# Optimization experiments

Measured on AMD Instinct MI355X. Metric: run time of the kernel, lower is better.

## Reference

```python
import jax, jax.numpy as jnp
import numpy as np

NUM_EXPERTS = 8
TOP_K = 2
DIM = 1024
HIDDEN = 4096
BATCH, SEQ = 16, 32


def setup_inputs() -> dict:
    key = jax.random.key(0)
    k1, k2, k3, k4, k5 = jax.random.split(key, 5)
    scale = 1.0 / np.sqrt(DIM)
    return {
        "hidden_states": jax.random.normal(k1, (BATCH, SEQ, DIM), dtype=jnp.float32),
        "gate_w": jax.random.normal(k2, (NUM_EXPERTS, DIM), dtype=jnp.float32) * scale,
        "w1": jax.random.normal(k3, (NUM_EXPERTS, HIDDEN, DIM), dtype=jnp.float32) * scale,
        "w3": jax.random.normal(k4, (NUM_EXPERTS, HIDDEN, DIM), dtype=jnp.float32) * scale,
        "w2": jax.random.normal(k5, (NUM_EXPERTS, DIM, HIDDEN), dtype=jnp.float32) * (1.0 / np.sqrt(HIDDEN)),
    }


def reference(hidden_states, gate_w, w1, w3, w2):
    B, S, D = hidden_states.shape
    x = hidden_states.reshape(-1, D)  # [T, D]

    # Router: softmax in fp32, top-k, renormalize (Mixtral style)
    router_logits = x @ gate_w.T  # [T, E]
    probs = jax.nn.softmax(router_logits.astype(jnp.float32), axis=-1)
    routing_weights, selected_experts = jax.lax.top_k(probs, TOP_K)  # [T, K]
    routing_weights = routing_weights / routing_weights.sum(axis=-1, keepdims=True)
    routing_weights = routing_weights.astype(x.dtype)

    # Per-token per-expert combine coefficient: coef[t, e] = sum_k w[t,k] * 1[sel[t,k]==e]
    coef = (jax.nn.one_hot(selected_experts, NUM_EXPERTS, dtype=x.dtype)
            * routing_weights[..., None]).sum(axis=1)  # [T, E]

    # SwiGLU FFN for all experts (grouped GEMM form), combined by coef.
    h1 = jnp.einsum('td,ehd->teh', x, w1)           # [T, E, H]
    h3 = jnp.einsum('td,ehd->teh', x, w3)           # [T, E, H]
    act = jax.nn.silu(h1) * h3                      # [T, E, H]
    expert_out = jnp.einsum('teh,edh->ted', act, w2)  # [T, E, D]
    out = jnp.einsum('ted,te->td', expert_out, coef)  # [T, D]
    return out.reshape(B, S, D)
```

## Files before the change

kernel.cpp:

```cpp
#include <hip/hip_runtime.h>
#include <hip/hip_bf16.h>

#define E_ 8
#define D_ 1024
#define H_ 4096
#define T_ 512
#define A_ 1024
#define BM_ 192

typedef __attribute__((ext_vector_type(8))) short bf16x8;
typedef __attribute__((ext_vector_type(4))) float f32x4;

__device__ __forceinline__ unsigned short f2bf(float f) {
  __hip_bfloat16 h = __float2bfloat16(f);
  return *reinterpret_cast<unsigned short*>(&h);
}

__device__ __forceinline__ bf16x8 pk8(float4 a, float4 b) {
  bf16x8 r;
  r[0] = (short)f2bf(a.x); r[1] = (short)f2bf(a.y);
  r[2] = (short)f2bf(a.z); r[3] = (short)f2bf(a.w);
  r[4] = (short)f2bf(b.x); r[5] = (short)f2bf(b.y);
  r[6] = (short)f2bf(b.z); r[7] = (short)f2bf(b.w);
  return r;
}

__device__ __forceinline__ void gl16(const void* g, void* l) {
  __builtin_amdgcn_global_load_lds(
      (const __attribute__((address_space(1))) unsigned int*)g,
      (__attribute__((address_space(3))) unsigned int*)l, 16, 0, 0);
}

__global__ void moe_router(const float* __restrict__ x,
                           const float* __restrict__ gw,
                           unsigned short* __restrict__ xb,
                           int* __restrict__ sel,
                           float* __restrict__ wtop) {
  const int t = blockIdx.x;
  const int lane = threadIdx.x;
  const float* xr = x + (size_t)t * D_;

  float4 xv[4];
#pragma unroll
  for (int i = 0; i < 4; ++i) xv[i] = *reinterpret_cast<const float4*>(xr + (i * 64 + lane) * 4);
#pragma unroll
  for (int i = 0; i < 4; ++i) {
    ushort4 u;
    u.x = f2bf(xv[i].x); u.y = f2bf(xv[i].y); u.z = f2bf(xv[i].z); u.w = f2bf(xv[i].w);
    *reinterpret_cast<ushort4*>(xb + (size_t)t * D_ + (i * 64 + lane) * 4) = u;
  }

  float lg[E_];
  for (int e = 0; e < E_; ++e) {
    const float* g = gw + (size_t)e * D_;
    float p = 0.f;
#pragma unroll
    for (int i = 0; i < 4; ++i) {
      float4 gv = *reinterpret_cast<const float4*>(g + (i * 64 + lane) * 4);
      p += xv[i].x * gv.x + xv[i].y * gv.y + xv[i].z * gv.z + xv[i].w * gv.w;
    }
#pragma unroll
    for (int off = 32; off; off >>= 1) p += __shfl_xor(p, off);
    lg[e] = p;
  }
  if (lane == 0) {
    float m = lg[0];
    for (int e = 1; e < E_; ++e) m = fmaxf(m, lg[e]);
    float pr[E_];
    float s = 0.f;
    for (int e = 0; e < E_; ++e) { pr[e] = __expf(lg[e] - m); s += pr[e]; }
    const float inv = 1.f / s;
    for (int e = 0; e < E_; ++e) pr[e] *= inv;
    float v0 = -1.f, v1 = -1.f; int i0 = 0, i1 = 0;
    for (int e = 0; e < E_; ++e) {
      float p = pr[e];
      if (p > v0)      { v1 = v0; i1 = i0; v0 = p; i0 = e; }
      else if (p > v1) { v1 = p; i1 = e; }
    }
    const float s2 = 1.f / (v0 + v1);
    sel[2 * t] = i0; sel[2 * t + 1] = i1;
    wtop[2 * t] = v0 * s2; wtop[2 * t + 1] = v1 * s2;
  }
}

__global__ void moe_compact(const int* __restrict__ sel,
                            const float* __restrict__ wtop,
                            int* __restrict__ counts,
                            int* __restrict__ offsets,
                            int* __restrict__ tok,
                            int* __restrict__ slotof,
                            float* __restrict__ coef) {
  const int tid = threadIdx.x;
  const int e = tid >> 6;
  const int lane = tid & 63;
  __shared__ int cnt[E_], offs[E_];

  int base = 0;
  for (int c = 0; c < T_ / 64; ++c) {
    const int t = c * 64 + lane;
    const bool f = (sel[2 * t] == e) || (sel[2 * t + 1] == e);
    base += __popcll(__ballot(f));
  }
  if (lane == 0) cnt[e] = base;
  __syncthreads();
  if (tid == 0) {
    int o = 0;
    for (int i = 0; i < E_; ++i) { offs[i] = o; o += cnt[i]; }
  }
  __syncthreads();
  if (lane == 0) { counts[e] = cnt[e]; offsets[e] = offs[e]; }

  int pos = offs[e];
  for (int c = 0; c < T_ / 64; ++c) {
    const int t = c * 64 + lane;
    const int s0 = sel[2 * t], s1 = sel[2 * t + 1];
    const bool f = (s0 == e) || (s1 == e);
    unsigned long long b = __ballot(f);
    const int myp = pos + __popcll(b & ((1ull << lane) - 1ull));
    if (f) {
      const int k = (s0 == e) ? 0 : 1;
      tok[myp] = t;
      slotof[2 * t + k] = myp;
      coef[myp] = wtop[2 * t + k];
    }
    pos += __popcll(b);
  }
}


#define STAGE1(buf, kt) do {                                                  \
    _Pragma("unroll")                                                         \
    for (int j = 0; j < 3; ++j)                                               \
      gl16(asrc[j] + (kt), &As[buf][(j * 4 + wid) * 512]);                    \
    _Pragma("unroll")                                                         \
    for (int j = 0; j < 2; ++j) {                                             \
      gl16(b1src[j] + (kt), &B1s[buf][(j * 4 + wid) * 256]);                  \
      gl16(b3src[j] + (kt), &B3s[buf][(j * 4 + wid) * 256]);                  \
    }                                                                         \
  } while (0)

__launch_bounds__(256, 2)
__global__ void moe_ffn1(const unsigned short* __restrict__ xb,
                         const float* __restrict__ w1,
                         const float* __restrict__ w3,
                         const int* __restrict__ counts,
                         const int* __restrict__ offsets,
                         const int* __restrict__ tok,
                         unsigned short* __restrict__ act) {
  const int bid = blockIdx.x;
  const int hg = bid & 63;
  const int e = bid >> 6;
  const int count = counts[e];
  const int off = offsets[e];
  const int hbase = hg * 64;

  __shared__ unsigned short As[2][BM_ * 32];
  __shared__ float B1s[2][64 * 32];
  __shared__ float B3s[2][64 * 32];

  const int tid = threadIdx.x;
  const int lane = tid & 63, wid = tid >> 6;
  const int lr = lane & 15, kg = lane >> 4;
  const int wm = wid * 48;

  const int cA = (((lane & 3) ^ ((lane >> 3) & 3)) << 3);
  const int cB = (((lane & 7) ^ ((lane >> 3) & 7)) << 2);
  const float* b1src[2];
  const float* b3src[2];
#pragma unroll
  for (int j = 0; j < 2; ++j) {
    const int row = (j * 4 + wid) * 8 + (lane >> 3);
    b1src[j] = w1 + ((size_t)e * H_ + hbase + row) * D_ + cB;
    b3src[j] = w3 + ((size_t)e * H_ + hbase + row) * D_ + cB;
  }

  for (int m0 = 0; m0 < count; m0 += BM_) {
    const unsigned short* asrc[3];
#pragma unroll
    for (int j = 0; j < 3; ++j) {
      const int row = (j * 4 + wid) * 16 + (lane >> 2);
      const int cr = (m0 + row < count) ? (m0 + row) : (count - 1);
      asrc[j] = xb + (size_t)tok[off + cr] * D_ + cA;
    }
    const int q = count - m0 - wm;
    const int mfn = (q <= 0) ? 0 : ((q + 15) >> 4 < 3 ? (q + 15) >> 4 : 3);

    f32x4 acc1[3][4] = {};
    f32x4 acc3[3][4] = {};

    STAGE1(0, 0);
    __syncthreads();

    int cur = 0;
    const int pa = ((kg ^ ((lr >> 1) & 3)) << 3);
    const int q0 = (((kg * 2) ^ (lr & 7)) << 2);
    const int q1 = (((kg * 2 + 1) ^ (lr & 7)) << 2);
    for (int it = 0; it < 32; ++it) {
      if (it + 1 < 32) STAGE1(cur ^ 1, (it + 1) * 32);
      bf16x8 af[3];
#pragma unroll
      for (int mf = 0; mf < 3; ++mf)
        af[mf] = *reinterpret_cast<const bf16x8*>(&As[cur][(wm + mf * 16 + lr) * 32 + pa]);
#pragma unroll
      for (int nf = 0; nf < 4; ++nf) {
        const int rb = (nf * 16 + lr) * 32;
        bf16x8 b1f = pk8(*reinterpret_cast<const float4*>(&B1s[cur][rb + q0]),
                         *reinterpret_cast<const float4*>(&B1s[cur][rb + q1]));
        bf16x8 b3f = pk8(*reinterpret_cast<const float4*>(&B3s[cur][rb + q0]),
                         *reinterpret_cast<const float4*>(&B3s[cur][rb + q1]));
#pragma unroll
        for (int mf = 0; mf < 3; ++mf)
          if (mf < mfn) {
            acc1[mf][nf] = __builtin_amdgcn_mfma_f32_16x16x32_bf16(af[mf], b1f, acc1[mf][nf], 0, 0, 0);
            acc3[mf][nf] = __builtin_amdgcn_mfma_f32_16x16x32_bf16(af[mf], b3f, acc3[mf][nf], 0, 0, 0);
          }
      }
      if (it + 1 < 32) { __syncthreads(); cur ^= 1; }
    }

#pragma unroll
    for (int mf = 0; mf < 3; ++mf) {
#pragma unroll
      for (int r = 0; r < 4; ++r) {
        const int mrow = m0 + wm + mf * 16 + kg * 4 + r;
        if (mrow < count) {
          const size_t rb = (size_t)(off + mrow) * H_;
#pragma unroll
          for (int nf = 0; nf < 4; ++nf) {
            const float h1 = acc1[mf][nf][r];
            const float h3 = acc3[mf][nf][r];
            const float a = h1 / (1.f + __expf(-h1)) * h3;
            act[rb + hbase + nf * 16 + lr] = f2bf(a);
          }
        }
      }
    }
    __syncthreads();
  }
}

#define STAGE2(buf, kt) do {                                                  \
    _Pragma("unroll")                                                         \
    for (int j = 0; j < 3; ++j)                                               \
      gl16(asrc[j] + (kt), &As[buf][(j * 4 + wid) * 512]);                    \
    _Pragma("unroll")                                                         \
    for (int j = 0; j < 2; ++j)                                               \
      gl16(bsrc[j] + (kt), &Bs[buf][(j * 4 + wid) * 256]);                    \
  } while (0)

__launch_bounds__(256, 2)
__global__ void moe_ffn2(const unsigned short* __restrict__ act,
                         const float* __restrict__ w2,
                         const int* __restrict__ counts,
                         const int* __restrict__ offsets,
                         const float* __restrict__ coef,
                         float* __restrict__ part,
                         int kschunk) {
  const int bid = blockIdx.x;
  const int ks = bid >> 7;
  const int e = (bid >> 4) & 7;
  const int dg = bid & 15;
  const int count = counts[e];
  const int off = offsets[e];
  const int dbase = dg * 64;
  const int kbase = ks * kschunk;
  const int nit = kschunk >> 5;

  __shared__ unsigned short As[2][BM_ * 32];
  __shared__ float Bs[2][64 * 32];

  const int tid = threadIdx.x;
  const int lane = tid & 63, wid = tid >> 6;
  const int lr = lane & 15, kg = lane >> 4;
  const int wm = wid * 48;

  const int cA = (((lane & 3) ^ ((lane >> 3) & 3)) << 3);
  const int cB = (((lane & 7) ^ ((lane >> 3) & 7)) << 2);
  const float* bsrc[2];
#pragma unroll
  for (int j = 0; j < 2; ++j) {
    const int row = (j * 4 + wid) * 8 + (lane >> 3);
    bsrc[j] = w2 + ((size_t)e * D_ + dbase + row) * H_ + kbase + cB;
  }

  for (int m0 = 0; m0 < count; m0 += BM_) {
    const unsigned short* asrc[3];
#pragma unroll
    for (int j = 0; j < 3; ++j) {
      const int row = (j * 4 + wid) * 16 + (lane >> 2);
      const int cr = (m0 + row < count) ? (m0 + row) : (count - 1);
      asrc[j] = act + (size_t)(off + cr) * H_ + kbase + cA;
    }
    const int q = count - m0 - wm;
    const int mfn = (q <= 0) ? 0 : ((q + 15) >> 4 < 3 ? (q + 15) >> 4 : 3);

    f32x4 acc[3][4] = {};

    STAGE2(0, 0);
    __syncthreads();

    int cur = 0;
    const int pa = ((kg ^ ((lr >> 1) & 3)) << 3);
    const int q0 = (((kg * 2) ^ (lr & 7)) << 2);
    const int q1 = (((kg * 2 + 1) ^ (lr & 7)) << 2);
    for (int it = 0; it < nit; ++it) {
      if (it + 1 < nit) STAGE2(cur ^ 1, (it + 1) * 32);
      bf16x8 af[3];
#pragma unroll
      for (int mf = 0; mf < 3; ++mf)
        af[mf] = *reinterpret_cast<const bf16x8*>(&As[cur][(wm + mf * 16 + lr) * 32 + pa]);
#pragma unroll
      for (int nf = 0; nf < 4; ++nf) {
        const int rb = (nf * 16 + lr) * 32;
        bf16x8 bf = pk8(*reinterpret_cast<const float4*>(&Bs[cur][rb + q0]),
                        *reinterpret_cast<const float4*>(&Bs[cur][rb + q1]));
#pragma unroll
        for (int mf = 0; mf < 3; ++mf)
          if (mf < mfn)
            acc[mf][nf] = __builtin_amdgcn_mfma_f32_16x16x32_bf16(af[mf], bf, acc[mf][nf], 0, 0, 0);
      }
      if (it + 1 < nit) { __syncthreads(); cur ^= 1; }
    }

#pragma unroll
    for (int mf = 0; mf < 3; ++mf) {
#pragma unroll
      for (int r = 0; r < 4; ++r) {
        const int mrow = m0 + wm + mf * 16 + kg * 4 + r;
        if (mrow < count) {
          const float cf = coef[off + mrow];
          float* prow = part + ((size_t)ks * A_ + off + mrow) * D_;
#pragma unroll
          for (int nf = 0; nf < 4; ++nf)
            prow[dbase + nf * 16 + lr] = cf * acc[mf][nf][r];
        }
      }
    }
    __syncthreads();
  }
}

__global__ void moe_combine(const float* __restrict__ part,
                            const int* __restrict__ slotof,
                            float* __restrict__ out,
                            int ksn) {
  const int t = blockIdx.x;
  const int i = threadIdx.x;
  const int g0 = slotof[2 * t], g1 = slotof[2 * t + 1];
  float4 o = make_float4(0.f, 0.f, 0.f, 0.f);
  for (int ks = 0; ks < ksn; ++ks) {
    const float* p = part + (size_t)ks * A_ * D_;
    float4 a = reinterpret_cast<const float4*>(p + (size_t)g0 * D_)[i];
    float4 b = reinterpret_cast<const float4*>(p + (size_t)g1 * D_)[i];
    o.x += a.x + b.x; o.y += a.y + b.y; o.z += a.z + b.z; o.w += a.w + b.w;
  }
  reinterpret_cast<float4*>(out + (size_t)t * D_)[i] = o;
}

extern "C" void kernel_launch(void* const* d_in, const int* in_sizes, int n_in,
                              void* d_out, int out_size, void* d_ws, size_t ws_size,
                              hipStream_t stream) {
  const float* x  = (const float*)d_in[0];
  const float* gw = (const float*)d_in[1];
  const float* w1 = (const float*)d_in[2];
  const float* w3 = (const float*)d_in[3];
  const float* w2 = (const float*)d_in[4];
  float* out = (float*)d_out;

  char* ws = (char*)d_ws;
  const size_t SM   = 32768;
  const size_t ACT  = (size_t)A_ * H_ * 2;
  const size_t XB   = (size_t)T_ * D_ * 2;
  const size_t P1   = (size_t)A_ * D_ * 4;

  char* sm = ws;
  unsigned short* act = (unsigned short*)(ws + SM);
  unsigned short* xb  = (unsigned short*)(ws + SM + ACT);
  float* part         = (float*)(ws + SM + ACT + XB);
  const size_t base = SM + ACT + XB;
  const int ksn = (ws_size >= base + 4 * P1) ? 4 : (ws_size >= base + 2 * P1) ? 2 : 1;

  int*   sel     = (int*)  (sm);
  float* wtop    = (float*)(sm + 4096);
  int*   counts  = (int*)  (sm + 8192);
  int*   offsets = (int*)  (sm + 8192 + 64);
  int*   tokl    = (int*)  (sm + 12288);
  int*   slotof  = (int*)  (sm + 16384);
  float* coef    = (float*)(sm + 20480);

  moe_router <<<T_, 64, 0, stream>>>(x, gw, xb, sel, wtop);
  moe_compact<<<1, 512, 0, stream>>>(sel, wtop, counts, offsets, tokl, slotof, coef);
  moe_ffn1   <<<E_ * 64, 256, 0, stream>>>(xb, w1, w3, counts, offsets, tokl, act);
  moe_ffn2   <<<128 * ksn, 256, 0, stream>>>(act, w2, counts, offsets, coef, part, H_ / ksn);
  moe_combine<<<T_, 256, 0, stream>>>(part, slotof, out, ksn);
}
```

Before: 144.9 us.

## Triple-buffer weight tiles, load activations directly to registers, interleave experts

Both FFN kernels stop staging the activation/token tile in shared memory. Each lane now reads its A fragments straight from global memory into registers. Weight tiles use a 3-stage ring buffer with manual vmcnt waits and a single barrier per iteration, replacing the double buffer with two syncthreads. Block indexing is changed so adjacent blocks belong to different experts, occupancy bounds are raised, and ffn2 may use 8 K-splits when workspace allows. The risks are hand-counted vmcnt values that could race if the compiler reorders loads, uncoalesced direct A reads, and a larger partial buffer for combine to reduce.

```diff
diff --git a/kernel.cpp b/kernel.cpp
--- a/kernel.cpp
+++ b/kernel.cpp
@@ -7,6 +7,7 @@
 #define T_ 512
 #define A_ 1024
 #define BM_ 192
+#define NBUF 3
 
 typedef __attribute__((ext_vector_type(8))) short bf16x8;
 typedef __attribute__((ext_vector_type(4))) float f32x4;
@@ -128,18 +129,21 @@
 }
 
 
-#define STAGE1(buf, kt) do {                                                  \
-    _Pragma("unroll")                                                         \
-    for (int j = 0; j < 3; ++j)                                               \
-      gl16(asrc[j] + (kt), &As[buf][(j * 4 + wid) * 512]);                    \
-    _Pragma("unroll")                                                         \
-    for (int j = 0; j < 2; ++j) {                                             \
-      gl16(b1src[j] + (kt), &B1s[buf][(j * 4 + wid) * 256]);                  \
-      gl16(b3src[j] + (kt), &B3s[buf][(j * 4 + wid) * 256]);                  \
-    }                                                                         \
+#define WAITS(it, nit)                                                        \
+    if ((it) == 0)              asm volatile("s_waitcnt vmcnt(4)" ::: "memory"); \
+    else if ((it) == (nit) - 1) asm volatile("s_waitcnt vmcnt(3)" ::: "memory"); \
+    else                        asm volatile("s_waitcnt vmcnt(7)" ::: "memory"); \
+    __builtin_amdgcn_s_barrier();                                             \
+    __builtin_amdgcn_sched_barrier(0);
+
+#define STAGE1(s, kt) do {                                                    \
+    gl16(b1src[0] + (kt), &B1s[s][wid * 256]);                                \
+    gl16(b1src[1] + (kt), &B1s[s][1024 + wid * 256]);                         \
+    gl16(b3src[0] + (kt), &B3s[s][wid * 256]);                                \
+    gl16(b3src[1] + (kt), &B3s[s][1024 + wid * 256]);                         \
   } while (0)
 
-__launch_bounds__(256, 2)
+__launch_bounds__(256, 3)
 __global__ void moe_ffn1(const unsigned short* __restrict__ xb,
                          const float* __restrict__ w1,
                          const float* __restrict__ w3,
@@ -148,23 +152,21 @@
                          const int* __restrict__ tok,
                          unsigned short* __restrict__ act) {
   const int bid = blockIdx.x;
-  const int hg = bid & 63;
-  const int e = bid >> 6;
+  const int e = bid & 7;
+  const int hg = bid >> 3;
   const int count = counts[e];
   const int off = offsets[e];
   const int hbase = hg * 64;
 
-  __shared__ unsigned short As[2][BM_ * 32];
-  __shared__ float B1s[2][64 * 32];
-  __shared__ float B3s[2][64 * 32];
+  __shared__ float B1s[NBUF][64 * 32];
+  __shared__ float B3s[NBUF][64 * 32];
 
   const int tid = threadIdx.x;
   const int lane = tid & 63, wid = tid >> 6;
   const int lr = lane & 15, kg = lane >> 4;
   const int wm = wid * 48;
 
-  const int cA = (((lane & 3) ^ ((lane >> 3) & 3)) << 3);
-  const int cB = (((lane & 7) ^ ((lane >> 3) & 7)) << 2);
+  const int cB = (((lane & 7) ^ (lane >> 3)) << 2);
   const float* b1src[2];
   const float* b3src[2];
 #pragma unroll
@@ -173,34 +175,40 @@
     b1src[j] = w1 + ((size_t)e * H_ + hbase + row) * D_ + cB;
     b3src[j] = w3 + ((size_t)e * H_ + hbase + row) * D_ + cB;
   }
+  const int q0 = (((2 * kg) ^ (lr & 7)) << 2);
+  const int q1 = (((2 * kg + 1) ^ (lr & 7)) << 2);
 
   for (int m0 = 0; m0 < count; m0 += BM_) {
-    const unsigned short* asrc[3];
-#pragma unroll
-    for (int j = 0; j < 3; ++j) {
-      const int row = (j * 4 + wid) * 16 + (lane >> 2);
-      const int cr = (m0 + row < count) ? (m0 + row) : (count - 1);
-      asrc[j] = xb + (size_t)tok[off + cr] * D_ + cA;
-    }
-    const int q = count - m0 - wm;
-    const int mfn = (q <= 0) ? 0 : ((q + 15) >> 4 < 3 ? (q + 15) >> 4 : 3);
+    const unsigned short* ap[3];
+#pragma unroll
+    for (int mf = 0; mf < 3; ++mf) {
+      const int row = m0 + wm + mf * 16 + lr;
+      const int cr = (row < count) ? row : (count - 1);
+      ap[mf] = xb + (size_t)tok[off + cr] * D_ + kg * 8;
+    }
+    const int qq = count - m0 - wm;
+    const int mfn = (qq <= 0) ? 0 : ((qq + 15) >> 4 < 3 ? (qq + 15) >> 4 : 3);
 
     f32x4 acc1[3][4] = {};
     f32x4 acc3[3][4] = {};
 
     STAGE1(0, 0);
-    __syncthreads();
+    STAGE1(1, 32);
 
     int cur = 0;
-    const int pa = ((kg ^ ((lr >> 1) & 3)) << 3);
-    const int q0 = (((kg * 2) ^ (lr & 7)) << 2);
-    const int q1 = (((kg * 2 + 1) ^ (lr & 7)) << 2);
     for (int it = 0; it < 32; ++it) {
-      if (it + 1 < 32) STAGE1(cur ^ 1, (it + 1) * 32);
+      WAITS(it, 32);
+
       bf16x8 af[3];
 #pragma unroll
       for (int mf = 0; mf < 3; ++mf)
-        af[mf] = *reinterpret_cast<const bf16x8*>(&As[cur][(wm + mf * 16 + lr) * 32 + pa]);
+        af[mf] = *reinterpret_cast<const bf16x8*>(ap[mf] + it * 32);
+
+      if (it + 2 < 32) {
+        int s2 = cur + 2; if (s2 >= NBUF) s2 -= NBUF;
+        STAGE1(s2, (it + 2) * 32);
+      }
+
 #pragma unroll
       for (int nf = 0; nf < 4; ++nf) {
         const int rb = (nf * 16 + lr) * 32;
@@ -215,7 +223,7 @@
             acc3[mf][nf] = __builtin_amdgcn_mfma_f32_16x16x32_bf16(af[mf], b3f, acc3[mf][nf], 0, 0, 0);
           }
       }
-      if (it + 1 < 32) { __syncthreads(); cur ^= 1; }
+      ++cur; if (cur >= NBUF) cur -= NBUF;
     }
 
 #pragma unroll
@@ -239,16 +247,12 @@
   }
 }
 
-#define STAGE2(buf, kt) do {                                                  \
-    _Pragma("unroll")                                                         \
-    for (int j = 0; j < 3; ++j)                                               \
-      gl16(asrc[j] + (kt), &As[buf][(j * 4 + wid) * 512]);                    \
-    _Pragma("unroll")                                                         \
-    for (int j = 0; j < 2; ++j)                                               \
-      gl16(bsrc[j] + (kt), &Bs[buf][(j * 4 + wid) * 256]);                    \
+#define STAGE2(s, kt) do {                                                    \
+    gl16(bsrc[0] + (kt), &Bs[s][wid * 256]);                                  \
+    gl16(bsrc[1] + (kt), &Bs[s][1024 + wid * 256]);                           \
   } while (0)
 
-__launch_bounds__(256, 2)
+__launch_bounds__(256, 4)
 __global__ void moe_ffn2(const unsigned short* __restrict__ act,
                          const float* __restrict__ w2,
                          const int* __restrict__ counts,
@@ -257,58 +261,63 @@
                          float* __restrict__ part,
                          int kschunk) {
   const int bid = blockIdx.x;
-  const int ks = bid >> 7;
-  const int e = (bid >> 4) & 7;
-  const int dg = bid & 15;
+  const int e = bid & 7;
+  const int r2 = bid >> 3;
+  const int dg = r2 & 15;
+  const int ks = r2 >> 4;
   const int count = counts[e];
   const int off = offsets[e];
   const int dbase = dg * 64;
   const int kbase = ks * kschunk;
   const int nit = kschunk >> 5;
 
-  __shared__ unsigned short As[2][BM_ * 32];
-  __shared__ float Bs[2][64 * 32];
+  __shared__ float Bs[NBUF][64 * 32];
 
   const int tid = threadIdx.x;
   const int lane = tid & 63, wid = tid >> 6;
   const int lr = lane & 15, kg = lane >> 4;
   const int wm = wid * 48;
 
-  const int cA = (((lane & 3) ^ ((lane >> 3) & 3)) << 3);
-  const int cB = (((lane & 7) ^ ((lane >> 3) & 7)) << 2);
+  const int cB = (((lane & 7) ^ (lane >> 3)) << 2);
   const float* bsrc[2];
 #pragma unroll
   for (int j = 0; j < 2; ++j) {
     const int row = (j * 4 + wid) * 8 + (lane >> 3);
     bsrc[j] = w2 + ((size_t)e * D_ + dbase + row) * H_ + kbase + cB;
   }
+  const int q0 = (((2 * kg) ^ (lr & 7)) << 2);
+  const int q1 = (((2 * kg + 1) ^ (lr & 7)) << 2);
 
   for (int m0 = 0; m0 < count; m0 += BM_) {
-    const unsigned short* asrc[3];
-#pragma unroll
-    for (int j = 0; j < 3; ++j) {
-      const int row = (j * 4 + wid) * 16 + (lane >> 2);
-      const int cr = (m0 + row < count) ? (m0 + row) : (count - 1);
-      asrc[j] = act + (size_t)(off + cr) * H_ + kbase + cA;
-    }
-    const int q = count - m0 - wm;
-    const int mfn = (q <= 0) ? 0 : ((q + 15) >> 4 < 3 ? (q + 15) >> 4 : 3);
+    const unsigned short* ap[3];
+#pragma unroll
+    for (int mf = 0; mf < 3; ++mf) {
+      const int row = m0 + wm + mf * 16 + lr;
+      const int cr = (row < count) ? row : (count - 1);
+      ap[mf] = act + (size_t)(off + cr) * H_ + kbase + kg * 8;
+    }
+    const int qq = count - m0 - wm;
+    const int mfn = (qq <= 0) ? 0 : ((qq + 15) >> 4 < 3 ? (qq + 15) >> 4 : 3);
 
     f32x4 acc[3][4] = {};
 
     STAGE2(0, 0);
-    __syncthreads();
+    STAGE2(1, 32);
 
     int cur = 0;
-    const int pa = ((kg ^ ((lr >> 1) & 3)) << 3);
-    const int q0 = (((kg * 2) ^ (lr & 7)) << 2);
-    const int q1 = (((kg * 2 + 1) ^ (lr & 7)) << 2);
     for (int it = 0; it < nit; ++it) {
-      if (it + 1 < nit) STAGE2(cur ^ 1, (it + 1) * 32);
+      WAITS(it, nit);
+
       bf16x8 af[3];
 #pragma unroll
       for (int mf = 0; mf < 3; ++mf)
-        af[mf] = *reinterpret_cast<const bf16x8*>(&As[cur][(wm + mf * 16 + lr) * 32 + pa]);
+        af[mf] = *reinterpret_cast<const bf16x8*>(ap[mf] + it * 32);
+
+      if (it + 2 < nit) {
+        int s2 = cur + 2; if (s2 >= NBUF) s2 -= NBUF;
+        STAGE2(s2, (it + 2) * 32);
+      }
+
 #pragma unroll
       for (int nf = 0; nf < 4; ++nf) {
         const int rb = (nf * 16 + lr) * 32;
@@ -319,7 +328,7 @@
           if (mf < mfn)
             acc[mf][nf] = __builtin_amdgcn_mfma_f32_16x16x32_bf16(af[mf], bf, acc[mf][nf], 0, 0, 0);
       }
-      if (it + 1 < nit) { __syncthreads(); cur ^= 1; }
+      ++cur; if (cur >= NBUF) cur -= NBUF;
     }
 
 #pragma unroll
@@ -378,7 +387,9 @@
   unsigned short* xb  = (unsigned short*)(ws + SM + ACT);
   float* part         = (float*)(ws + SM + ACT + XB);
   const size_t base = SM + ACT + XB;
-  const int ksn = (ws_size >= base + 4 * P1) ? 4 : (ws_size >= base + 2 * P1) ? 2 : 1;
+  const int ksn = (ws_size >= base + 8 * P1) ? 8 :
+                  (ws_size >= base + 4 * P1) ? 4 :
+                  (ws_size >= base + 2 * P1) ? 2 : 1;
 
   int*   sel     = (int*)  (sm);
   float* wtop    = (float*)(sm + 4096);
@@ -391,6 +402,6 @@
   moe_router <<<T_, 64, 0, stream>>>(x, gw, xb, sel, wtop);
   moe_compact<<<1, 512, 0, stream>>>(sel, wtop, counts, offsets, tokl, slotof, coef);
   moe_ffn1   <<<E_ * 64, 256, 0, stream>>>(xb, w1, w3, counts, offsets, tokl, act);
-  moe_ffn2   <<<128 * ksn, 256, 0, stream>>>(act, w2, counts, offsets, coef, part, H_ / ksn);
+  moe_ffn2   <<<E_ * 16 * ksn, 256, 0, stream>>>(act, w2, counts, offsets, coef, part, H_ / ksn);
   moe_combine<<<T_, 256, 0, stream>>>(part, slotof, out, ksn);
 }
```

New measurement: 143.3 us. No clear change (-1.1%).

## Rewrite ffn2 staging as register-staged loads with bf16 B tile and padded LDS

Applied to the files above, without the earlier changes.

Replaces the double-buffered direct global-to-LDS async copies in the down-projection kernel with a single-buffered scheme. Each K-step of 64 loads act and fp32 w2 into registers, converts w2 to bf16 once before writing it to shared memory, and stores both tiles into padded row-major LDS arrays instead of XOR-swizzled ones. It also returns early for experts with no tokens. This removes the repeated per-wave fp32-to-bf16 conversion of B fragments and halves B tile LDS footprint, but loses the overlap between the next tile's loads and the current tile's MFMAs, and adds two barriers per step.

```diff
diff --git a/kernel.cpp b/kernel.cpp
--- a/kernel.cpp
+++ b/kernel.cpp
@@ -7,9 +7,11 @@
 #define T_ 512
 #define A_ 1024
 #define BM_ 192
+#define LDA_ 72
 
 typedef __attribute__((ext_vector_type(8))) short bf16x8;
 typedef __attribute__((ext_vector_type(4))) float f32x4;
+typedef __attribute__((ext_vector_type(8))) unsigned short u16x8;
 
 __device__ __forceinline__ unsigned short f2bf(float f) {
   __hip_bfloat16 h = __float2bfloat16(f);
@@ -22,6 +24,13 @@
   r[2] = (short)f2bf(a.z); r[3] = (short)f2bf(a.w);
   r[4] = (short)f2bf(b.x); r[5] = (short)f2bf(b.y);
   r[6] = (short)f2bf(b.z); r[7] = (short)f2bf(b.w);
+  return r;
+}
+
+__device__ __forceinline__ u16x8 pack8(float4 a, float4 b) {
+  u16x8 r;
+  r[0] = f2bf(a.x); r[1] = f2bf(a.y); r[2] = f2bf(a.z); r[3] = f2bf(a.w);
+  r[4] = f2bf(b.x); r[5] = f2bf(b.y); r[6] = f2bf(b.z); r[7] = f2bf(b.w);
   return r;
 }
 
@@ -239,15 +248,6 @@
   }
 }
 
-#define STAGE2(buf, kt) do {                                                  \
-    _Pragma("unroll")                                                         \
-    for (int j = 0; j < 3; ++j)                                               \
-      gl16(asrc[j] + (kt), &As[buf][(j * 4 + wid) * 512]);                    \
-    _Pragma("unroll")                                                         \
-    for (int j = 0; j < 2; ++j)                                               \
-      gl16(bsrc[j] + (kt), &Bs[buf][(j * 4 + wid) * 256]);                    \
-  } while (0)
-
 __launch_bounds__(256, 2)
 __global__ void moe_ffn2(const unsigned short* __restrict__ act,
                          const float* __restrict__ w2,
@@ -261,65 +261,68 @@
   const int e = (bid >> 4) & 7;
   const int dg = bid & 15;
   const int count = counts[e];
+  if (count <= 0) return;
   const int off = offsets[e];
-  const int dbase = dg * 64;
   const int kbase = ks * kschunk;
-  const int nit = kschunk >> 5;
-
-  __shared__ unsigned short As[2][BM_ * 32];
-  __shared__ float Bs[2][64 * 32];
+
+  __shared__ unsigned short As[BM_][LDA_];
+  __shared__ unsigned short Bs[64][LDA_];
 
   const int tid = threadIdx.x;
   const int lane = tid & 63, wid = tid >> 6;
   const int lr = lane & 15, kg = lane >> 4;
   const int wm = wid * 48;
-
-  const int cA = (((lane & 3) ^ ((lane >> 3) & 3)) << 3);
-  const int cB = (((lane & 7) ^ ((lane >> 3) & 7)) << 2);
-  const float* bsrc[2];
-#pragma unroll
-  for (int j = 0; j < 2; ++j) {
-    const int row = (j * 4 + wid) * 8 + (lane >> 3);
-    bsrc[j] = w2 + ((size_t)e * D_ + dbase + row) * H_ + kbase + cB;
-  }
+  const int dbase = dg * 64;
+
+  const int brow = tid >> 2, bcol = (tid & 3) * 16;
+  const float* W2p = w2 + ((size_t)e * D_ + dbase + brow) * H_ + kbase + bcol;
 
   for (int m0 = 0; m0 < count; m0 += BM_) {
-    const unsigned short* asrc[3];
-#pragma unroll
-    for (int j = 0; j < 3; ++j) {
-      const int row = (j * 4 + wid) * 16 + (lane >> 2);
-      const int cr = (m0 + row < count) ? (m0 + row) : (count - 1);
-      asrc[j] = act + (size_t)(off + cr) * H_ + kbase + cA;
-    }
-    const int q = count - m0 - wm;
+    const int mc = count - m0;
+    const unsigned short* arow[6];
+#pragma unroll
+    for (int i = 0; i < 6; ++i) {
+      const int r = i * 32 + (tid >> 3);
+      const int cr = (m0 + r < count) ? (m0 + r) : (count - 1);
+      arow[i] = act + (size_t)(off + cr) * H_ + kbase + (tid & 7) * 8;
+    }
+    const int q = mc - wm;
     const int mfn = (q <= 0) ? 0 : ((q + 15) >> 4 < 3 ? (q + 15) >> 4 : 3);
 
     f32x4 acc[3][4] = {};
 
-    STAGE2(0, 0);
-    __syncthreads();
-
-    int cur = 0;
-    const int pa = ((kg ^ ((lr >> 1) & 3)) << 3);
-    const int q0 = (((kg * 2) ^ (lr & 7)) << 2);
-    const int q1 = (((kg * 2 + 1) ^ (lr & 7)) << 2);
-    for (int it = 0; it < nit; ++it) {
-      if (it + 1 < nit) STAGE2(cur ^ 1, (it + 1) * 32);
-      bf16x8 af[3];
-#pragma unroll
-      for (int mf = 0; mf < 3; ++mf)
-        af[mf] = *reinterpret_cast<const bf16x8*>(&As[cur][(wm + mf * 16 + lr) * 32 + pa]);
-#pragma unroll
-      for (int nf = 0; nf < 4; ++nf) {
-        const int rb = (nf * 16 + lr) * 32;
-        bf16x8 bf = pk8(*reinterpret_cast<const float4*>(&Bs[cur][rb + q0]),
-                        *reinterpret_cast<const float4*>(&Bs[cur][rb + q1]));
+    for (int kt = 0; kt < kschunk; kt += 64) {
+      __syncthreads();
+      u16x8 av[6];
+#pragma unroll
+      for (int i = 0; i < 6; ++i) av[i] = *reinterpret_cast<const u16x8*>(arow[i] + kt);
+      float4 bv[4];
+#pragma unroll
+      for (int i = 0; i < 4; ++i) bv[i] = *reinterpret_cast<const float4*>(W2p + kt + i * 4);
+#pragma unroll
+      for (int i = 0; i < 6; ++i)
+        *reinterpret_cast<u16x8*>(&As[i * 32 + (tid >> 3)][(tid & 7) * 8]) = av[i];
+#pragma unroll
+      for (int i = 0; i < 2; ++i)
+        *reinterpret_cast<u16x8*>(&Bs[brow][bcol + i * 8]) = pack8(bv[2 * i], bv[2 * i + 1]);
+      __syncthreads();
+
+#pragma unroll
+      for (int ks2 = 0; ks2 < 2; ++ks2) {
+        const int kc = ks2 * 32 + kg * 8;
+        bf16x8 af[3];
 #pragma unroll
         for (int mf = 0; mf < 3; ++mf)
-          if (mf < mfn)
-            acc[mf][nf] = __builtin_amdgcn_mfma_f32_16x16x32_bf16(af[mf], bf, acc[mf][nf], 0, 0, 0);
+          af[mf] = *reinterpret_cast<const bf16x8*>(&As[wm + mf * 16 + lr][kc]);
+#pragma unroll
+        for (int nf = 0; nf < 4; ++nf) {
+          bf16x8 bf = *reinterpret_cast<const bf16x8*>(&Bs[nf * 16 + lr][kc]);
+#pragma unroll
+          for (int mf = 0; mf < 3; ++mf)
+            if (mf < mfn)
+              acc[mf][nf] = __builtin_amdgcn_mfma_f32_16x16x32_bf16(af[mf], bf, acc[mf][nf], 0, 0, 0);
+        }
       }
-      if (it + 1 < nit) { __syncthreads(); cur ^= 1; }
     }
 
 #pragma unroll
@@ -336,7 +339,6 @@
         }
       }
     }
-    __syncthreads();
   }
 }
 
```

After: 128.6 us. 1.13x faster.
